# Kernel optimization log

Hardware: AMD Instinct MI355X
Metric: run time of the kernel (lower is better)

The kernel has to match this reference:

```python
import jax, jax.numpy as jnp
import numpy as np

N = 10000      # nodes
E = 160000     # edges
D_IN = 512
D_H = 512
P_DROP = 0.2


def _glorot(key, shape):
    lim = float(np.sqrt(6.0 / (shape[0] + shape[1])))
    return jax.random.uniform(key, shape, jnp.float32, -lim, lim)


def setup_inputs() -> dict:
    key = jax.random.key(0)
    ks = jax.random.split(key, 8)
    h = jax.random.normal(ks[0], (N, D_IN), jnp.float32)
    src = jax.random.randint(ks[1], (E,), 0, N)
    dst = jax.random.randint(ks[2], (E,), 0, N)
    edge_weight = jax.random.uniform(ks[3], (E,), jnp.float32)
    W0 = _glorot(ks[4], (D_IN, D_H))
    W1 = _glorot(ks[5], (D_H, D_H))
    W2 = _glorot(ks[6], (D_H, D_H))
    b0 = jnp.zeros((D_H,), jnp.float32)
    b1 = jnp.zeros((D_H,), jnp.float32)
    b2 = jnp.zeros((D_H,), jnp.float32)
    return dict(h=h, src=src, dst=dst, edge_weight=edge_weight,
                W0=W0, b0=b0, W1=W1, b1=b1, W2=W2, b2=b2)


def _dropout(x, key):
    keep = jax.random.bernoulli(key, 1.0 - P_DROP, x.shape)
    return jnp.where(keep, x / (1.0 - P_DROP), 0.0)


def _graph_conv(x, src, dst, ew, W, b, act):
    # DGL GraphConv, norm='both', weight=True, bias=True, with edge_weight.
    ones = jnp.ones((src.shape[0],), x.dtype)
    deg_out = jnp.maximum(jax.ops.segment_sum(ones, src, num_segments=N), 1.0)
    deg_in = jnp.maximum(jax.ops.segment_sum(ones, dst, num_segments=N), 1.0)
    x = x * (deg_out ** -0.5)[:, None]          # src norm
    msg = x[src] * ew[:, None]                  # [E, D] gather + edge weight
    agg = jax.ops.segment_sum(msg, dst, num_segments=N)  # scatter-add
    out = (agg @ W) * (deg_in ** -0.5)[:, None] + b
    return act(out) if act is not None else out


def reference(h, src, dst, edge_weight, W0, b0, W1, b1, W2, b2):
    dk = jax.random.split(jax.random.key(42), 3)
    x = _dropout(h, dk[0])
    x = _graph_conv(x, src, dst, edge_weight, W0, b0, jax.nn.elu)
    x = _dropout(x, dk[1])
    x = _graph_conv(x, src, dst, edge_weight, W1, b1, jax.nn.elu)
    x = _dropout(x, dk[2])
    x = _graph_conv(x, src, dst, edge_weight, W2, b2, None)
    return x
```

## Files before the change

kernel.cpp:

```cpp
#include <hip/hip_runtime.h>
#include <stdint.h>

#define N_NODES 10000
#define N_EDGES 160000
#define D 512
#define TOT (N_NODES * D)
#define NMASK (TOT / 32)
#define CAP 64
#define LDF 520

typedef _Float16 h8 __attribute__((ext_vector_type(8)));
typedef float f4 __attribute__((ext_vector_type(4)));

__host__ __device__ inline uint32_t rotl32(uint32_t v, int r) {
    return (v << r) | (v >> (32 - r));
}

__host__ __device__ inline void tf2x32(uint32_t k0, uint32_t k1,
                                       uint32_t& x0, uint32_t& x1) {
    uint32_t k2 = k0 ^ k1 ^ 0x1BD11BDAu;
    x0 += k0; x1 += k1;
    x0 += x1; x1 = rotl32(x1, 13); x1 ^= x0;
    x0 += x1; x1 = rotl32(x1, 15); x1 ^= x0;
    x0 += x1; x1 = rotl32(x1, 26); x1 ^= x0;
    x0 += x1; x1 = rotl32(x1,  6); x1 ^= x0;
    x0 += k1; x1 += k2 + 1u;
    x0 += x1; x1 = rotl32(x1, 17); x1 ^= x0;
    x0 += x1; x1 = rotl32(x1, 29); x1 ^= x0;
    x0 += x1; x1 = rotl32(x1, 16); x1 ^= x0;
    x0 += x1; x1 = rotl32(x1, 24); x1 ^= x0;
    x0 += k2; x1 += k0 + 2u;
    x0 += x1; x1 = rotl32(x1, 13); x1 ^= x0;
    x0 += x1; x1 = rotl32(x1, 15); x1 ^= x0;
    x0 += x1; x1 = rotl32(x1, 26); x1 ^= x0;
    x0 += x1; x1 = rotl32(x1,  6); x1 ^= x0;
    x0 += k0; x1 += k1 + 3u;
    x0 += x1; x1 = rotl32(x1, 17); x1 ^= x0;
    x0 += x1; x1 = rotl32(x1, 29); x1 ^= x0;
    x0 += x1; x1 = rotl32(x1, 16); x1 ^= x0;
    x0 += x1; x1 = rotl32(x1, 24); x1 ^= x0;
    x0 += k1; x1 += k2 + 4u;
    x0 += x1; x1 = rotl32(x1, 13); x1 ^= x0;
    x0 += x1; x1 = rotl32(x1, 15); x1 ^= x0;
    x0 += x1; x1 = rotl32(x1, 26); x1 ^= x0;
    x0 += x1; x1 = rotl32(x1,  6); x1 ^= x0;
    x0 += k2; x1 += k0 + 5u;
}

__device__ __forceinline__ uint32_t dropout_bit(uint32_t k0, uint32_t k1, uint32_t j) {
    uint32_t c0 = 0u, c1 = j;
    tf2x32(k0, k1, c0, c1);
    uint32_t bits = c0 ^ c1;
    float u = __uint_as_float((bits >> 9) | 0x3f800000u) - 1.0f;
    return (u < 0.8f) ? 1u : 0u;
}

#define HIST_BLKS 625
#define WCONV_BLKS 192
#define DROP_BLKS 5000
#define MASKG_BLKS 625
#define PRE_BLKS (HIST_BLKS + WCONV_BLKS + DROP_BLKS + 2 * MASKG_BLKS)
__global__ __launch_bounds__(256)
void pre_kernel(const int* __restrict__ src, int* __restrict__ deg_out,
                const float* __restrict__ W0, const float* __restrict__ W1,
                const float* __restrict__ W2, _Float16* __restrict__ Wt,
                const float* __restrict__ x, _Float16* __restrict__ y,
                uint32_t k0, uint32_t k1,
                uint32_t m1k0, uint32_t m1k1, uint32_t* __restrict__ mask1,
                uint32_t m2k0, uint32_t m2k1, uint32_t* __restrict__ mask2) {
    __shared__ float tile[64][65];
    int b = blockIdx.x;
    int t = threadIdx.x;
    if (b < HIST_BLKS) {
        int e = b * 256 + t;
        atomicAdd(&deg_out[src[e]], 1);
    } else if (b < HIST_BLKS + WCONV_BLKS) {
        int b2 = b - HIST_BLKS;
        int bx = b2 & 7, by = (b2 >> 3) & 7, bz = b2 >> 6;
        const float* W = (bz == 0) ? W0 : (bz == 1) ? W1 : W2;
        _Float16* T = Wt + (size_t)bz * 512 * 512;
        int r0 = by * 64, c0 = bx * 64;
        int c = t & 63, rq = t >> 6;
#pragma unroll
        for (int i = 0; i < 16; ++i) {
            int r = rq + i * 4;
            tile[r][c] = W[(size_t)(r0 + r) * 512 + c0 + c];
        }
        __syncthreads();
        int k = t & 63, nq = t >> 6;
#pragma unroll
        for (int i = 0; i < 16; ++i) {
            int n = nq + i * 4;
            T[(size_t)(c0 + n) * 512 + r0 + k] = (_Float16)tile[k][n];
        }
    } else if (b < HIST_BLKS + WCONV_BLKS + DROP_BLKS) {
        int b3 = b - HIST_BLKS - WCONV_BLKS;
        int j = (b3 * 256 + t) * 4;
        if (j >= TOT) return;
        float4 xv = *(const float4*)&x[j];
        _Float16 r[4];
        uint32_t jj = (uint32_t)j;
#pragma unroll
        for (int i = 0; i < 4; ++i) {
            float g = dropout_bit(k0, k1, jj + (uint32_t)i) ? 1.0f : 0.0f;
            float xi = (&xv.x)[i];
            r[i] = (_Float16)(g * (xi * 1.25f));
        }
        *(ushort4*)&y[j] = *(ushort4*)r;
    } else {
        int b4 = b - HIST_BLKS - WCONV_BLKS - DROP_BLKS;
        int which = b4 / MASKG_BLKS;
        int gtid = (b4 % MASKG_BLKS) * 256 + t;
        uint32_t mk0 = which ? m2k0 : m1k0;
        uint32_t mk1 = which ? m2k1 : m1k1;
        uint32_t* m = which ? mask2 : mask1;
        uint32_t w = 0, jb = (uint32_t)gtid * 32u;
#pragma unroll 4
        for (int i = 0; i < 32; ++i)
            w |= dropout_bit(mk0, mk1, jb + (uint32_t)i) << i;
        m[gtid] = w;
    }
}

__global__ __launch_bounds__(256)
void fill_kernel(const int* __restrict__ src, const int* __restrict__ dst,
                 const float* __restrict__ ew, const int* __restrict__ deg_out,
                 int* __restrict__ cnt_in, int2* __restrict__ ell) {
    int e = blockIdx.x * 256 + threadIdx.x;
    int v = dst[e];
    int sn = src[e];
    int pos = atomicAdd(&cnt_in[v], 1);
    float rno = 1.0f / sqrtf(fmaxf((float)deg_out[sn], 1.0f));
    if (pos < CAP)
        ell[(size_t)v * CAP + pos] = make_int2(sn, __float_as_int(ew[e] * rno));
}

__global__ __launch_bounds__(256)
void fused_layer(const _Float16* __restrict__ yin, const int* __restrict__ cnt_in,
                 const int2* __restrict__ ell, const _Float16* __restrict__ Wt,
                 const float* __restrict__ bias, const uint32_t* __restrict__ mask,
                 _Float16* __restrict__ yout, float* __restrict__ fout, int mode) {
    __shared__ _Float16 AT[16 * LDF];
    const int tid = threadIdx.x;
    const int w = tid >> 6, lane = tid & 63;
    const int base = blockIdx.x * 16;
    const _Float16* yl = yin + lane * 8;

    for (int i = 0; i < 4; ++i) {
        int row = w * 4 + i;
        int node = base + row;
        int deg = cnt_in[node];
        if (deg > CAP) deg = CAP;
        const int2* ep = ell + (size_t)node * CAP;
        float acc[8] = {0, 0, 0, 0, 0, 0, 0, 0};
        int k = 0;
        for (; k + 15 < deg; k += 16) {
            int2 e[16];
#pragma unroll
            for (int u = 0; u < 16; ++u) e[u] = ep[k + u];
            h8 v[16];
#pragma unroll
            for (int u = 0; u < 16; ++u) v[u] = *(const h8*)&yl[(size_t)e[u].x * 512];
#pragma unroll
            for (int u = 0; u < 16; ++u) {
                float wt = __int_as_float(e[u].y);
#pragma unroll
                for (int j = 0; j < 8; ++j) acc[j] += wt * (float)v[u][j];
            }
        }
        for (; k + 3 < deg; k += 4) {
            int2 e[4];
#pragma unroll
            for (int u = 0; u < 4; ++u) e[u] = ep[k + u];
            h8 v[4];
#pragma unroll
            for (int u = 0; u < 4; ++u) v[u] = *(const h8*)&yl[(size_t)e[u].x * 512];
#pragma unroll
            for (int u = 0; u < 4; ++u) {
                float wt = __int_as_float(e[u].y);
#pragma unroll
                for (int j = 0; j < 8; ++j) acc[j] += wt * (float)v[u][j];
            }
        }
        for (; k < deg; ++k) {
            int2 e0 = ep[k];
            float wt = __int_as_float(e0.y);
            h8 v = *(const h8*)&yl[(size_t)e0.x * 512];
#pragma unroll
            for (int j = 0; j < 8; ++j) acc[j] += wt * (float)v[j];
        }
        _Float16 r[8];
#pragma unroll
        for (int j = 0; j < 8; ++j) r[j] = (_Float16)acc[j];
        *(h8*)&AT[row * LDF + lane * 8] = *(h8*)r;
    }
    __syncthreads();

    h8 a[16];
#pragma unroll
    for (int ks = 0; ks < 16; ++ks)
        a[ks] = *(const h8*)&AT[(lane & 15) * LDF + ks * 32 + (lane >> 4) * 8];
    __syncthreads();

    const int r0 = (lane >> 4) * 4;
    float rn[4];
#pragma unroll
    for (int i = 0; i < 4; ++i) {
        int d = cnt_in[base + r0 + i];
        rn[i] = 1.0f / sqrtf(fmaxf((float)d, 1.0f));
    }

    const _Float16* bp = Wt + (size_t)(lane & 15) * 512 + (lane >> 4) * 8;

    h8 bfA[16], bfB[16];
    auto bload = [&](h8* d, int nt) {
        const _Float16* bn = bp + (size_t)nt * (16 * 512);
#pragma unroll
        for (int ks = 0; ks < 16; ++ks) d[ks] = *(const h8*)(bn + ks * 32);
    };
    auto mmaepi = [&](const h8* bf, int nt) {
        f4 c0 = (f4){0.f, 0.f, 0.f, 0.f}, c1 = c0, c2 = c0, c3 = c0;
#pragma unroll
        for (int q = 0; q < 4; ++q) {
            c0 = __builtin_amdgcn_mfma_f32_16x16x32_f16(a[q],      bf[q],      c0, 0, 0, 0);
            c1 = __builtin_amdgcn_mfma_f32_16x16x32_f16(a[4 + q],  bf[4 + q],  c1, 0, 0, 0);
            c2 = __builtin_amdgcn_mfma_f32_16x16x32_f16(a[8 + q],  bf[8 + q],  c2, 0, 0, 0);
            c3 = __builtin_amdgcn_mfma_f32_16x16x32_f16(a[12 + q], bf[12 + q], c3, 0, 0, 0);
        }
        f4 c = (c0 + c1) + (c2 + c3);
        int col = nt * 16 + (lane & 15);
        float bcol = bias[col];
#pragma unroll
        for (int i = 0; i < 4; ++i) {
            int gr = base + r0 + i;
            float v = c[i] * rn[i] + bcol;
            if (mode == 0) {
                v = (v > 0.f) ? v : (__expf(v) - 1.0f);
                uint32_t j = (uint32_t)(gr * 512 + col);
                uint32_t g = (mask[j >> 5] >> (j & 31)) & 1u;
                v = g ? (v * 1.25f) : 0.0f;
                AT[(r0 + i) * LDF + col] = (_Float16)v;
            } else {
                fout[(size_t)gr * 512 + col] = v;
            }
        }
    };

    const int nt0 = w * 8;
    bload(bfA, nt0);
#pragma unroll 1
    for (int j = 0; j < 8; j += 2) {
        bload(bfB, nt0 + j + 1);
        mmaepi(bfA, nt0 + j);
        if (j + 2 < 8) bload(bfA, nt0 + j + 2);
        mmaepi(bfB, nt0 + j + 1);
    }

    if (mode == 0) {
        __syncthreads();
#pragma unroll
        for (int i = 0; i < 4; ++i) {
            int c = tid + 256 * i;
            int row = c >> 6, col8 = c & 63;
            *(h8*)&yout[(size_t)(base + row) * 512 + col8 * 8] =
                *(const h8*)&AT[row * LDF + col8 * 8];
        }
    }
}

extern "C" void kernel_launch(void* const* d_in, const int* in_sizes, int n_in,
                              void* d_out, int out_size, void* d_ws, size_t ws_size,
                              hipStream_t stream) {
    const float* x   = (const float*)d_in[0];
    const int*   src = (const int*)d_in[1];
    const int*   dst = (const int*)d_in[2];
    const float* ew  = (const float*)d_in[3];
    const float* W0  = (const float*)d_in[4];
    const float* b0  = (const float*)d_in[5];
    const float* W1  = (const float*)d_in[6];
    const float* b1  = (const float*)d_in[7];
    const float* W2  = (const float*)d_in[8];
    const float* b2  = (const float*)d_in[9];
    float* out = (float*)d_out;

    char* ws = (char*)d_ws;
    _Float16* y16  = (_Float16*)ws; ws += (size_t)TOT * 2;
    _Float16* y16b = (_Float16*)ws; ws += (size_t)TOT * 2;
    _Float16* Wt   = (_Float16*)ws; ws += (size_t)3 * 512 * 512 * 2;
    int* deg_out = (int*)ws;   ws += N_NODES * 4;
    int* cnt_in  = (int*)ws;   ws += N_NODES * 4;
    ws = (char*)(((uintptr_t)ws + 15) & ~(uintptr_t)15);
    int2* ell    = (int2*)ws;  ws += (size_t)N_NODES * CAP * 8;
    uint32_t* mask1 = (uint32_t*)ws; ws += (size_t)NMASK * 4;
    uint32_t* mask2 = (uint32_t*)ws; ws += (size_t)NMASK * 4;

    uint32_t dk[3][2];
    for (int i = 0; i < 3; ++i) {
        uint32_t c0 = 0u, c1 = (uint32_t)i;
        tf2x32(0u, 42u, c0, c1);
        dk[i][0] = c0; dk[i][1] = c1;
    }

    hipMemsetAsync(deg_out, 0, 2 * N_NODES * 4, stream);

    pre_kernel<<<PRE_BLKS, 256, 0, stream>>>(src, deg_out, W0, W1, W2, Wt,
                                             x, y16, dk[0][0], dk[0][1],
                                             dk[1][0], dk[1][1], mask1,
                                             dk[2][0], dk[2][1], mask2);
    fill_kernel<<<N_EDGES / 256, 256, 0, stream>>>(src, dst, ew, deg_out,
                                                   cnt_in, ell);

    fused_layer<<<625, 256, 0, stream>>>(y16, cnt_in, ell, Wt,
                                         b0, mask1, y16b, nullptr, 0);
    fused_layer<<<625, 256, 0, stream>>>(y16b, cnt_in, ell, Wt + (size_t)512 * 512,
                                         b1, mask2, y16, nullptr, 0);
    fused_layer<<<625, 256, 0, stream>>>(y16, cnt_in, ell, Wt + (size_t)2 * 512 * 512,
                                         b2, nullptr, nullptr, out, 1);
}
```

Before: 378.2 us.

## Use 32-row tiles with 512 threads and stage weights through shared memory

```diff
diff --git a/kernel.cpp b/kernel.cpp
--- a/kernel.cpp
+++ b/kernel.cpp
@@ -7,7 +7,10 @@
 #define TOT (N_NODES * D)
 #define NMASK (TOT / 32)
 #define CAP 64
-#define LDF 520
+#define MT 32
+#define NBLK_F 313
+#define LDA3 520
+#define LDB 40
 
 typedef _Float16 h8 __attribute__((ext_vector_type(8)));
 typedef float f4 __attribute__((ext_vector_type(4)));
@@ -135,21 +138,22 @@
         ell[(size_t)v * CAP + pos] = make_int2(sn, __float_as_int(ew[e] * rno));
 }
 
-__global__ __launch_bounds__(256)
+__global__ __launch_bounds__(512, 4)
 void fused_layer(const _Float16* __restrict__ yin, const int* __restrict__ cnt_in,
                  const int2* __restrict__ ell, const _Float16* __restrict__ Wt,
                  const float* __restrict__ bias, const uint32_t* __restrict__ mask,
                  _Float16* __restrict__ yout, float* __restrict__ fout, int mode) {
-    __shared__ _Float16 AT[16 * LDF];
+    __shared__ _Float16 AT[MT * LDA3];
+    __shared__ _Float16 Bs[512 * LDB];
     const int tid = threadIdx.x;
     const int w = tid >> 6, lane = tid & 63;
-    const int base = blockIdx.x * 16;
+    const int base = blockIdx.x * MT;
     const _Float16* yl = yin + lane * 8;
 
     for (int i = 0; i < 4; ++i) {
         int row = w * 4 + i;
         int node = base + row;
-        int deg = cnt_in[node];
+        int deg = (node < N_NODES) ? cnt_in[node] : 0;
         if (deg > CAP) deg = CAP;
         const int2* ep = ell + (size_t)node * CAP;
         float acc[8] = {0, 0, 0, 0, 0, 0, 0, 0};
@@ -192,78 +196,86 @@
         _Float16 r[8];
 #pragma unroll
         for (int j = 0; j < 8; ++j) r[j] = (_Float16)acc[j];
-        *(h8*)&AT[row * LDF + lane * 8] = *(h8*)r;
+        *(h8*)&AT[row * LDA3 + lane * 8] = *(h8*)r;
     }
     __syncthreads();
 
-    h8 a[16];
-#pragma unroll
-    for (int ks = 0; ks < 16; ++ks)
-        a[ks] = *(const h8*)&AT[(lane & 15) * LDF + ks * 32 + (lane >> 4) * 8];
-    __syncthreads();
-
-    const int r0 = (lane >> 4) * 4;
+    const int mq = w & 1, nq = w >> 1;
+    f4 acc[8];
+#pragma unroll
+    for (int i = 0; i < 8; ++i) acc[i] = (f4){0.f, 0.f, 0.f, 0.f};
+
+    const _Float16* wrow = Wt + (size_t)tid * 512;
+    _Float16* bw = &Bs[tid * LDB];
+    const _Float16* arow = &AT[(mq * 16 + (lane & 15)) * LDA3 + (lane >> 4) * 8];
+    const _Float16* brow = &Bs[(nq * 128 + (lane & 15)) * LDB + (lane >> 4) * 8];
+
+    h8 rb0 = *(const h8*)(wrow + 0);
+    h8 rb1 = *(const h8*)(wrow + 8);
+    h8 rb2 = *(const h8*)(wrow + 16);
+    h8 rb3 = *(const h8*)(wrow + 24);
+
+    for (int ks = 0; ks < 16; ++ks) {
+        *(h8*)(bw + 0)  = rb0;
+        *(h8*)(bw + 8)  = rb1;
+        *(h8*)(bw + 16) = rb2;
+        *(h8*)(bw + 24) = rb3;
+        __syncthreads();
+        if (ks < 15) {
+            const _Float16* nx = wrow + (ks + 1) * 32;
+            rb0 = *(const h8*)(nx + 0);
+            rb1 = *(const h8*)(nx + 8);
+            rb2 = *(const h8*)(nx + 16);
+            rb3 = *(const h8*)(nx + 24);
+        }
+        h8 a = *(const h8*)(arow + ks * 32);
+#pragma unroll
+        for (int nt = 0; nt < 8; ++nt) {
+            h8 bf = *(const h8*)(brow + nt * 16 * LDB);
+            acc[nt] = __builtin_amdgcn_mfma_f32_16x16x32_f16(a, bf, acc[nt], 0, 0, 0);
+        }
+        __syncthreads();
+    }
+
+    const int r0g = (lane >> 4) * 4;
     float rn[4];
 #pragma unroll
     for (int i = 0; i < 4; ++i) {
-        int d = cnt_in[base + r0 + i];
+        int gr = base + mq * 16 + r0g + i;
+        int d = (gr < N_NODES) ? cnt_in[gr] : 1;
         rn[i] = 1.0f / sqrtf(fmaxf((float)d, 1.0f));
     }
-
-    const _Float16* bp = Wt + (size_t)(lane & 15) * 512 + (lane >> 4) * 8;
-
-    h8 bfA[16], bfB[16];
-    auto bload = [&](h8* d, int nt) {
-        const _Float16* bn = bp + (size_t)nt * (16 * 512);
-#pragma unroll
-        for (int ks = 0; ks < 16; ++ks) d[ks] = *(const h8*)(bn + ks * 32);
-    };
-    auto mmaepi = [&](const h8* bf, int nt) {
-        f4 c0 = (f4){0.f, 0.f, 0.f, 0.f}, c1 = c0, c2 = c0, c3 = c0;
-#pragma unroll
-        for (int q = 0; q < 4; ++q) {
-            c0 = __builtin_amdgcn_mfma_f32_16x16x32_f16(a[q],      bf[q],      c0, 0, 0, 0);
-            c1 = __builtin_amdgcn_mfma_f32_16x16x32_f16(a[4 + q],  bf[4 + q],  c1, 0, 0, 0);
-            c2 = __builtin_amdgcn_mfma_f32_16x16x32_f16(a[8 + q],  bf[8 + q],  c2, 0, 0, 0);
-            c3 = __builtin_amdgcn_mfma_f32_16x16x32_f16(a[12 + q], bf[12 + q], c3, 0, 0, 0);
-        }
-        f4 c = (c0 + c1) + (c2 + c3);
-        int col = nt * 16 + (lane & 15);
+#pragma unroll
+    for (int nt = 0; nt < 8; ++nt) {
+        int col = nq * 128 + nt * 16 + (lane & 15);
         float bcol = bias[col];
 #pragma unroll
         for (int i = 0; i < 4; ++i) {
-            int gr = base + r0 + i;
-            float v = c[i] * rn[i] + bcol;
+            int gr = base + mq * 16 + r0g + i;
+            if (gr >= N_NODES) continue;
+            float v = acc[nt][i] * rn[i] + bcol;
             if (mode == 0) {
                 v = (v > 0.f) ? v : (__expf(v) - 1.0f);
                 uint32_t j = (uint32_t)(gr * 512 + col);
                 uint32_t g = (mask[j >> 5] >> (j & 31)) & 1u;
                 v = g ? (v * 1.25f) : 0.0f;
-                AT[(r0 + i) * LDF + col] = (_Float16)v;
+                AT[(mq * 16 + r0g + i) * LDA3 + col] = (_Float16)v;
             } else {
                 fout[(size_t)gr * 512 + col] = v;
             }
         }
-    };
-
-    const int nt0 = w * 8;
-    bload(bfA, nt0);
-#pragma unroll 1
-    for (int j = 0; j < 8; j += 2) {
-        bload(bfB, nt0 + j + 1);
-        mmaepi(bfA, nt0 + j);
-        if (j + 2 < 8) bload(bfA, nt0 + j + 2);
-        mmaepi(bfB, nt0 + j + 1);
     }
 
     if (mode == 0) {
         __syncthreads();
 #pragma unroll
         for (int i = 0; i < 4; ++i) {
-            int c = tid + 256 * i;
+            int c = tid + 512 * i;
             int row = c >> 6, col8 = c & 63;
-            *(h8*)&yout[(size_t)(base + row) * 512 + col8 * 8] =
-                *(const h8*)&AT[row * LDF + col8 * 8];
+            int gr = base + row;
+            if (gr < N_NODES)
+                *(h8*)&yout[(size_t)gr * 512 + col8 * 8] =
+                    *(const h8*)&AT[row * LDA3 + col8 * 8];
         }
     }
 }
@@ -310,10 +322,10 @@
     fill_kernel<<<N_EDGES / 256, 256, 0, stream>>>(src, dst, ew, deg_out,
                                                    cnt_in, ell);
 
-    fused_layer<<<625, 256, 0, stream>>>(y16, cnt_in, ell, Wt,
-                                         b0, mask1, y16b, nullptr, 0);
-    fused_layer<<<625, 256, 0, stream>>>(y16b, cnt_in, ell, Wt + (size_t)512 * 512,
-                                         b1, mask2, y16, nullptr, 0);
-    fused_layer<<<625, 256, 0, stream>>>(y16, cnt_in, ell, Wt + (size_t)2 * 512 * 512,
-                                         b2, nullptr, nullptr, out, 1);
-}
+    fused_layer<<<NBLK_F, 512, 0, stream>>>(y16, cnt_in, ell, Wt,
+                                            b0, mask1, y16b, nullptr, 0);
+    fused_layer<<<NBLK_F, 512, 0, stream>>>(y16b, cnt_in, ell, Wt + (size_t)512 * 512,
+                                            b1, mask2, y16, nullptr, 0);
+    fused_layer<<<NBLK_F, 512, 0, stream>>>(y16, cnt_in, ell, Wt + (size_t)2 * 512 * 512,
+                                            b2, nullptr, nullptr, out, 1);
+}
```

After: 325.3 us. -14.0%, faster.
